# Kernel tuning notes

Hardware: AMD Instinct MI355X
Metric: run time of the kernel (lower is better)

The kernel has to match this reference:

```python
import jax, jax.numpy as jnp
import numpy as np

N_NODES = 100000
N_EDGES = 3200000
D_IN = 64
D_OUT = 64


def setup_inputs() -> dict:
    key = jax.random.key(0)
    k0, k1, k2, k3 = jax.random.split(key, 4)
    x = jax.random.normal(k0, (N_NODES, D_IN), dtype=jnp.float32)
    edge_index = jax.random.randint(k1, (2, N_EDGES), 0, N_NODES, dtype=jnp.int64)
    edge_weight = jax.random.uniform(k2, (N_EDGES,), dtype=jnp.float32)
    W = jax.random.normal(k3, (D_IN, D_OUT), dtype=jnp.float32) / jnp.sqrt(jnp.float32(D_IN))
    b = jnp.zeros((D_OUT,), dtype=jnp.float32)
    return {"x": x, "edge_index": edge_index, "edge_weight": edge_weight, "W": W, "b": b}


def reference(x, edge_index, edge_weight, W, b):
    # GiGCNConv forward: asymmetric (random-walk, D^-1 A) gcn_norm with self loops,
    # then GCNConv(normalize=False): linear -> edge-weighted scatter-add -> bias.
    N = x.shape[0]
    src, dst = edge_index[0], edge_index[1]

    # add self loops (fill value 1.0 since improved=False)
    loop = jnp.arange(N, dtype=src.dtype)
    src = jnp.concatenate([src, loop])
    dst = jnp.concatenate([dst, loop])
    ew = jnp.concatenate([edge_weight.astype(x.dtype), jnp.ones((N,), dtype=x.dtype)])

    # asymmetric normalization: in-degree (at dst) inverse scaling
    deg = jax.ops.segment_sum(ew, dst, num_segments=N)          # [N]
    deg_inv = jnp.where(deg > 0, 1.0 / deg, 0.0)                # inf -> 0
    norm = deg_inv[dst] * ew                                    # [E+N]

    # GCNConv: project then aggregate messages at destination nodes
    h = x @ W                                                   # [N, D_OUT]
    msg = norm[:, None] * h[src]                                # [E+N, D_OUT] gather
    out = jax.ops.segment_sum(msg, dst, num_segments=N)         # scatter-add
    return out + b
```

## Files before the change

kernel.cpp:

```cpp
#include <hip/hip_runtime.h>


#define D 64
#define BSH 9
#define NPB 512
#define MAXB1 256
#define BATCHA 4096
#define C1S 32
#define WSCALE 8192.0f
#define WINV (1.0f / 8192.0f)

static __device__ __forceinline__ unsigned short f2bf(float f) {
    unsigned u = __float_as_uint(f);
    u += 0x7FFFu + ((u >> 16) & 1u);
    return (unsigned short)(u >> 16);
}
static __device__ __forceinline__ float bflo(unsigned u) {
    return __uint_as_float(u << 16);
}
static __device__ __forceinline__ float bfhi(unsigned u) {
    return __uint_as_float(u & 0xFFFF0000u);
}


__global__ __launch_bounds__(256) void hist_kernel(const int* __restrict__ dst,
                                                   int* __restrict__ hist, int E, int B1) {
    __shared__ int lh[MAXB1];
    int tid = threadIdx.x;
    if (tid < MAXB1) lh[tid] = 0;
    __syncthreads();
    int t = blockIdx.x * 256 + tid;
    int stride = gridDim.x * 256;
    if ((E & 3) == 0 && (((size_t)dst & 15) == 0)) {
        const int4* d4 = (const int4*)dst;
        int n4 = E >> 2;
        for (int e = t; e < n4; e += stride) {
            int4 v = d4[e];
            atomicAdd(&lh[v.x >> BSH], 1);
            atomicAdd(&lh[v.y >> BSH], 1);
            atomicAdd(&lh[v.z >> BSH], 1);
            atomicAdd(&lh[v.w >> BSH], 1);
        }
    } else {
        for (int e = t; e < E; e += stride) {
            int d = __builtin_nontemporal_load(dst + e);
            atomicAdd(&lh[d >> BSH], 1);
        }
    }
    __syncthreads();
    if (tid < B1) {
        int v = lh[tid];
        if (v) atomicAdd(&hist[tid], v);
    }
}


__global__ __launch_bounds__(256) void scan_kernel(const int* __restrict__ hist,
                                                   int* __restrict__ off1,
                                                   int* __restrict__ cur1, int B1, int E) {
    __shared__ int s[256];
    int tid = threadIdx.x;
    int v = (tid < B1) ? hist[tid] : 0;
    s[tid] = v;
    __syncthreads();
    for (int o = 1; o < 256; o <<= 1) {
        int t = (tid >= o) ? s[tid - o] : 0;
        __syncthreads();
        s[tid] += t;
        __syncthreads();
    }
    if (tid < B1) {
        int ex = s[tid] - v;
        off1[tid] = ex;
        cur1[tid * C1S] = ex;
    }
    if (tid == 0) off1[B1] = E;
}


__global__ __launch_bounds__(256) void partA_kernel(const int* __restrict__ src,
                                                    const int* __restrict__ dst,
                                                    const float* __restrict__ ew,
                                                    int* __restrict__ cur1,
                                                    int2* __restrict__ pairs1,
                                                    int E, int nb, int aligned) {
    __shared__ int bcnt[MAXB1];
    __shared__ int bbase[MAXB1];
    __shared__ int brank[MAXB1];
    int tid = threadIdx.x;
    for (int ib = blockIdx.x; ib < nb; ib += gridDim.x) {
        int base = ib * BATCHA;
        int blen = E - base;
        if (blen > BATCHA) blen = BATCHA;
        if (tid < MAXB1) { bcnt[tid] = 0; brank[tid] = 0; }
        __syncthreads();
        int dv[16], sv[16];
        float wv[16];
        int off = tid * 16;
        if (aligned && off + 16 <= blen) {
#pragma unroll
            for (int kk = 0; kk < 4; ++kk) {
                int4 d4 = ((const int4*)(dst + base + off))[kk];
                int4 s4 = ((const int4*)(src + base + off))[kk];
                float4 w4 = ((const float4*)(ew + base + off))[kk];
                dv[kk * 4 + 0] = d4.x; dv[kk * 4 + 1] = d4.y;
                dv[kk * 4 + 2] = d4.z; dv[kk * 4 + 3] = d4.w;
                sv[kk * 4 + 0] = s4.x; sv[kk * 4 + 1] = s4.y;
                sv[kk * 4 + 2] = s4.z; sv[kk * 4 + 3] = s4.w;
                wv[kk * 4 + 0] = w4.x; wv[kk * 4 + 1] = w4.y;
                wv[kk * 4 + 2] = w4.z; wv[kk * 4 + 3] = w4.w;
            }
#pragma unroll
            for (int m = 0; m < 16; ++m) atomicAdd(&bcnt[dv[m] >> BSH], 1);
        } else {
#pragma unroll
            for (int m = 0; m < 16; ++m) {
                bool v = (off + m) < blen;
                int e = base + off + m;
                dv[m] = v ? __builtin_nontemporal_load(dst + e) : -1;
                sv[m] = v ? __builtin_nontemporal_load(src + e) : 0;
                wv[m] = v ? __builtin_nontemporal_load(ew + e) : 0.0f;
                if (v) atomicAdd(&bcnt[dv[m] >> BSH], 1);
            }
        }
        __syncthreads();
        if (tid < MAXB1 && bcnt[tid] > 0)
            bbase[tid] = atomicAdd(&cur1[tid * C1S], bcnt[tid]);
        __syncthreads();
#pragma unroll
        for (int m = 0; m < 16; ++m) {
            if (dv[m] >= 0) {
                int bin = dv[m] >> BSH;
                int r = atomicAdd(&brank[bin], 1);
                pairs1[bbase[bin] + r] =
                    make_int2(sv[m] | ((dv[m] & (NPB - 1)) << 17),
                              __float_as_int(wv[m]));
            }
        }
        __syncthreads();
    }
}


__global__ __launch_bounds__(512) void sortmerge_kernel(const int2* __restrict__ pairs1,
                                                        const int* __restrict__ off1,
                                                        unsigned* __restrict__ cw,
                                                        int* __restrict__ node_off,
                                                        int N, int B1) {
    __shared__ int lh[NPB];
    __shared__ int s[NPB];
    __shared__ int cur[NPB];
    int tid = threadIdx.x;
    int c = blockIdx.x;
    int e0 = off1[c], e1 = off1[c + 1];

    lh[tid] = 0;
    __syncthreads();

    for (int ib = e0; ib < e1; ib += 512 * 8) {
        long long pv[8];
#pragma unroll
        for (int m = 0; m < 8; ++m) {
            int i = ib + m * 512 + tid;
            pv[m] = (i < e1)
                ? __builtin_nontemporal_load((const long long*)(pairs1 + i))
                : -1LL;
        }
#pragma unroll
        for (int m = 0; m < 8; ++m) {
            int i = ib + m * 512 + tid;
            if (i < e1) atomicAdd(&lh[((int)pv[m] >> 17) & (NPB - 1)], 1);
        }
    }
    __syncthreads();

    s[tid] = lh[tid];
    __syncthreads();
    for (int o = 1; o < NPB; o <<= 1) {
        int t = (tid >= o) ? s[tid - o] : 0;
        __syncthreads();
        s[tid] += t;
        __syncthreads();
    }
    int ex = s[tid] - lh[tid];
    int gbase = c << BSH;
    if (gbase + tid <= N) node_off[gbase + tid] = e0 + ex;
    if (c == B1 - 1 && tid == 0) node_off[N] = e1;
    cur[tid] = ex;
    __syncthreads();

    for (int ib = e0; ib < e1; ib += 512 * 8) {
        long long pv[8];
#pragma unroll
        for (int m = 0; m < 8; ++m) {
            int i = ib + m * 512 + tid;
            pv[m] = (i < e1)
                ? __builtin_nontemporal_load((const long long*)(pairs1 + i))
                : -1LL;
        }
#pragma unroll
        for (int m = 0; m < 8; ++m) {
            int i = ib + m * 512 + tid;
            if (i < e1) {
                int px = (int)pv[m];
                float w = __int_as_float((int)(pv[m] >> 32));
                int node = (px >> 17) & (NPB - 1);
                int pos = atomicAdd(&cur[node], 1);
                int wq = (int)fminf(fmaxf(w, 0.0f) * WSCALE + 0.5f, 32767.0f);
                cw[e0 + pos] = (unsigned)(px & 0x1FFFF) | ((unsigned)wq << 17);
            }
        }
    }
}


__global__ __launch_bounds__(256) void gemmW_kernel(const float* __restrict__ x,
                                                    const float* __restrict__ W,
                                                    unsigned short* __restrict__ hbf, int N) {
    __shared__ float Ws[D * D];
    __shared__ float xs[32][D];
    int tid = threadIdx.x;
    int j = tid & 63;
    int g = tid >> 6;
    int base = blockIdx.x * 32;
    for (int i = tid; i < D * D; i += 256) Ws[i] = W[i];
    for (int rr = g; rr < 32; rr += 4) {
        int r = base + rr;
        if (r < N) xs[rr][j] = x[(size_t)r * D + j];
    }
    __syncthreads();
    float wc[D];
#pragma unroll
    for (int k = 0; k < D; ++k) wc[k] = Ws[k * D + j];
    for (int rr = g; rr < 32; rr += 4) {
        int r = base + rr;
        if (r < N) {
            float s0 = 0.0f, s1 = 0.0f, s2 = 0.0f, s3 = 0.0f;
#pragma unroll
            for (int k = 0; k < D; k += 4) {
                s0 = fmaf(xs[rr][k + 0], wc[k + 0], s0);
                s1 = fmaf(xs[rr][k + 1], wc[k + 1], s1);
                s2 = fmaf(xs[rr][k + 2], wc[k + 2], s2);
                s3 = fmaf(xs[rr][k + 3], wc[k + 3], s3);
            }
            hbf[(size_t)r * D + j] = f2bf((s0 + s1) + (s2 + s3));
        }
    }
}


__global__ __launch_bounds__(256) void accum_kernel(const unsigned* __restrict__ cw,
                                                    const int* __restrict__ node_off,
                                                    const unsigned short* __restrict__ hbf,
                                                    const float* __restrict__ bias,
                                                    float* __restrict__ out, int N) {
    int t = blockIdx.x * 256 + threadIdx.x;
    int n = t >> 6;
    int l = t & 63;
    if (n >= N) return;
    int eg = l >> 4;
    int cl = l & 15;
    int base = node_off[n];
    int cnt = node_off[n + 1] - base;
    const unsigned* pp = cw + base;
    const unsigned short* hcol = hbf + cl * 4;

    float a0 = 0.0f, a1 = 0.0f, a2 = 0.0f, a3 = 0.0f;
    float degs = 0.0f;
    int i = eg;
    for (; i + 12 < cnt; i += 16) {
        unsigned va = pp[i];
        unsigned vb = pp[i + 4];
        unsigned vc = pp[i + 8];
        unsigned vd = pp[i + 12];
        uint2 ha = *(const uint2*)(hcol + (size_t)(va & 0x1FFFF) * D);
        uint2 hb = *(const uint2*)(hcol + (size_t)(vb & 0x1FFFF) * D);
        uint2 hc = *(const uint2*)(hcol + (size_t)(vc & 0x1FFFF) * D);
        uint2 hd = *(const uint2*)(hcol + (size_t)(vd & 0x1FFFF) * D);
        float wa = (float)(va >> 17) * WINV;
        float wb = (float)(vb >> 17) * WINV;
        float wc = (float)(vc >> 17) * WINV;
        float wd = (float)(vd >> 17) * WINV;
        degs += (wa + wb) + (wc + wd);
        a0 = fmaf(wa, bflo(ha.x), a0);
        a1 = fmaf(wa, bfhi(ha.x), a1);
        a2 = fmaf(wa, bflo(ha.y), a2);
        a3 = fmaf(wa, bfhi(ha.y), a3);
        a0 = fmaf(wb, bflo(hb.x), a0);
        a1 = fmaf(wb, bfhi(hb.x), a1);
        a2 = fmaf(wb, bflo(hb.y), a2);
        a3 = fmaf(wb, bfhi(hb.y), a3);
        a0 = fmaf(wc, bflo(hc.x), a0);
        a1 = fmaf(wc, bfhi(hc.x), a1);
        a2 = fmaf(wc, bflo(hc.y), a2);
        a3 = fmaf(wc, bfhi(hc.y), a3);
        a0 = fmaf(wd, bflo(hd.x), a0);
        a1 = fmaf(wd, bfhi(hd.x), a1);
        a2 = fmaf(wd, bflo(hd.y), a2);
        a3 = fmaf(wd, bfhi(hd.y), a3);
    }
    for (; i < cnt; i += 4) {
        unsigned v = pp[i];
        uint2 hv = *(const uint2*)(hcol + (size_t)(v & 0x1FFFF) * D);
        float w = (float)(v >> 17) * WINV;
        degs += w;
        a0 = fmaf(w, bflo(hv.x), a0);
        a1 = fmaf(w, bfhi(hv.x), a1);
        a2 = fmaf(w, bflo(hv.y), a2);
        a3 = fmaf(w, bfhi(hv.y), a3);
    }

    a0 += __shfl_xor(a0, 16); a0 += __shfl_xor(a0, 32);
    a1 += __shfl_xor(a1, 16); a1 += __shfl_xor(a1, 32);
    a2 += __shfl_xor(a2, 16); a2 += __shfl_xor(a2, 32);
    a3 += __shfl_xor(a3, 16); a3 += __shfl_xor(a3, 32);
    degs += __shfl_xor(degs, 16); degs += __shfl_xor(degs, 32);

    if (eg == 0) {
        uint2 hs = *(const uint2*)(hcol + (size_t)n * D);
        a0 += bflo(hs.x);
        a1 += bfhi(hs.x);
        a2 += bflo(hs.y);
        a3 += bfhi(hs.y);
        degs += 1.0f;
        float di = 1.0f / degs;
        const float4 bv = *(const float4*)(bias + cl * 4);
        float4 o;
        o.x = fmaf(di, a0, bv.x);
        o.y = fmaf(di, a1, bv.y);
        o.z = fmaf(di, a2, bv.z);
        o.w = fmaf(di, a3, bv.w);
        __builtin_nontemporal_store(o.x, out + (size_t)n * D + cl * 4 + 0);
        __builtin_nontemporal_store(o.y, out + (size_t)n * D + cl * 4 + 1);
        __builtin_nontemporal_store(o.z, out + (size_t)n * D + cl * 4 + 2);
        __builtin_nontemporal_store(o.w, out + (size_t)n * D + cl * 4 + 3);
    }
}


__global__ __launch_bounds__(256) void deg_kernel(const int* __restrict__ dst,
                                                  const float* __restrict__ ew,
                                                  float* __restrict__ deg, int E) {
    int t = blockIdx.x * 256 + threadIdx.x;
    int stride = gridDim.x * 256;
    for (int e = t; e < E; e += stride) atomicAdd(&deg[dst[e]], ew[e]);
}

__global__ __launch_bounds__(256) void deginv_kernel(float* __restrict__ deg, int N) {
    int t = blockIdx.x * 256 + threadIdx.x;
    int stride = gridDim.x * 256;
    for (int n = t; n < N; n += stride) {
        float tot = deg[n] + 1.0f;
        deg[n] = (tot > 0.0f) ? (1.0f / tot) : 0.0f;
    }
}

__global__ __launch_bounds__(256) void gemm16f_kernel(const float* __restrict__ x,
                                                      const float* __restrict__ W,
                                                      float* __restrict__ h, int N) {
    __shared__ float Ws[D * D];
    __shared__ float xs[16][D];
    int tid = threadIdx.x;
    int j = tid & 63;
    int q = tid >> 6;
    int base = blockIdx.x * 16;
    for (int i = tid; i < D * D; i += 256) Ws[i] = W[i];
    for (int rr = q; rr < 16; rr += 4) {
        int r = base + rr;
        if (r < N) xs[rr][j] = x[(size_t)r * D + j];
    }
    __syncthreads();
    for (int rr = q; rr < 16; rr += 4) {
        int r = base + rr;
        if (r < N) {
            float sum = 0.0f;
#pragma unroll
            for (int k = 0; k < D; ++k) sum = fmaf(xs[rr][k], Ws[k * D + j], sum);
            h[(size_t)r * D + j] = sum;
        }
    }
}

__global__ __launch_bounds__(256) void init_kernel(const float* __restrict__ h,
                                                   const float* __restrict__ deginv,
                                                   const float* __restrict__ b,
                                                   float* __restrict__ out, int N) {
    int t = blockIdx.x * 256 + threadIdx.x;
    int stride = gridDim.x * 256;
    int nq = N * (D / 4);
    const float4* h4 = (const float4*)h;
    const float4* b4 = (const float4*)b;
    float4* o4 = (float4*)out;
    for (int q = t; q < nq; q += stride) {
        int n = q >> 4;
        int c4 = q & 15;
        float4 hv = h4[q];
        float4 bv = b4[c4];
        float di = deginv[n];
        float4 o;
        o.x = bv.x + di * hv.x;
        o.y = bv.y + di * hv.y;
        o.z = bv.z + di * hv.z;
        o.w = bv.w + di * hv.w;
        o4[q] = o;
    }
}

__global__ __launch_bounds__(256) void scatter_kernel(const int* __restrict__ src,
                                                      const int* __restrict__ dst,
                                                      const float* __restrict__ ew,
                                                      const float* __restrict__ deginv,
                                                      const float* __restrict__ h,
                                                      float* __restrict__ out, int E) {
    int t = blockIdx.x * 256 + threadIdx.x;
    int wave = t >> 6;
    int lane = t & 63;
    int nwaves = (gridDim.x * 256) >> 6;
    for (int e = wave; e < E; e += nwaves) {
        int s = src[e];
        int d = dst[e];
        float norm = deginv[d] * ew[e];
        atomicAdd(&out[d * D + lane], norm * h[s * D + lane]);
    }
}


extern "C" void kernel_launch(void* const* d_in, const int* in_sizes, int n_in,
                              void* d_out, int out_size, void* d_ws, size_t ws_size,
                              hipStream_t stream) {
    const float* x  = (const float*)d_in[0];
    const int*   ei = (const int*)d_in[1];
    const float* ew = (const float*)d_in[2];
    const float* W  = (const float*)d_in[3];
    const float* b  = (const float*)d_in[4];
    float* out = (float*)d_out;

    int N = in_sizes[0] / D;
    int E = in_sizes[2];
    const int* srcp = ei;
    const int* dstp = ei + E;

    int B1 = (N + NPB - 1) >> BSH;

    size_t ints_n = 256 + 320 + (size_t)MAXB1 * C1S + ((size_t)N + 64);
    size_t p1_off  = ((ints_n * 4) + 255) & ~(size_t)255;
    size_t hbf_off = (p1_off + (size_t)E * 8 + 255) & ~(size_t)255;
    size_t cw_off  = (hbf_off + (size_t)N * D * 2 + 255) & ~(size_t)255;
    size_t need = cw_off + (size_t)E * 4;

    if (N <= 131072 && ws_size >= need) {
        int* hist     = (int*)d_ws;
        int* off1     = hist + 256;
        int* cur1     = off1 + 320;
        int* node_off = cur1 + (size_t)MAXB1 * C1S;
        int2* pairs1  = (int2*)((char*)d_ws + p1_off);
        unsigned short* hbf = (unsigned short*)((char*)d_ws + hbf_off);
        unsigned* cw  = (unsigned*)((char*)d_ws + cw_off);

        int aligned = (((E & 3) == 0) && (((size_t)dstp & 15) == 0)) ? 1 : 0;

        hipMemsetAsync(hist, 0, 256 * 4, stream);
        hist_kernel<<<512, 256, 0, stream>>>(dstp, hist, E, B1);
        scan_kernel<<<1, 256, 0, stream>>>(hist, off1, cur1, B1, E);
        int nb = (E + BATCHA - 1) / BATCHA;
        int gA = nb < 2048 ? nb : 2048;
        partA_kernel<<<gA, 256, 0, stream>>>(srcp, dstp, ew, cur1, pairs1, E, nb, aligned);
        sortmerge_kernel<<<B1, 512, 0, stream>>>(pairs1, off1, cw, node_off, N, B1);
        gemmW_kernel<<<(N + 31) / 32, 256, 0, stream>>>(x, W, hbf, N);
        accum_kernel<<<(N + 3) / 4, 256, 0, stream>>>(cw, node_off, hbf, b, out, N);
    } else {
        size_t Npad = ((size_t)N + 63) & ~(size_t)63;
        float* deg = (float*)d_ws;
        float* h = deg + Npad;
        hipMemsetAsync(deg, 0, (size_t)N * sizeof(float), stream);
        deg_kernel<<<2048, 256, 0, stream>>>(dstp, ew, deg, E);
        deginv_kernel<<<(N + 255) / 256, 256, 0, stream>>>(deg, N);
        gemm16f_kernel<<<(N + 15) / 16, 256, 0, stream>>>(x, W, h, N);
        init_kernel<<<2048, 256, 0, stream>>>(h, deg, b, out, N);
        scatter_kernel<<<2048, 256, 0, stream>>>(srcp, dstp, ew, deg, h, out, E);
    }
}
```

Baseline: 183.1 us.

## Merge edge partition and X·W GEMM into one heterogeneous launch

```diff
diff --git a/kernel.cpp b/kernel.cpp
--- a/kernel.cpp
+++ b/kernel.cpp
@@ -78,66 +78,101 @@
 }
 
 
-__global__ __launch_bounds__(256) void partA_kernel(const int* __restrict__ src,
-                                                    const int* __restrict__ dst,
-                                                    const float* __restrict__ ew,
-                                                    int* __restrict__ cur1,
-                                                    int2* __restrict__ pairs1,
-                                                    int E, int nb, int aligned) {
-    __shared__ int bcnt[MAXB1];
-    __shared__ int bbase[MAXB1];
-    __shared__ int brank[MAXB1];
+__global__ __launch_bounds__(256) void partgemm_kernel(const int* __restrict__ src,
+                                                       const int* __restrict__ dst,
+                                                       const float* __restrict__ ew,
+                                                       int* __restrict__ cur1,
+                                                       int2* __restrict__ pairs1,
+                                                       int E, int nb, int aligned, int gA,
+                                                       const float* __restrict__ x,
+                                                       const float* __restrict__ W,
+                                                       unsigned short* __restrict__ hbf,
+                                                       int N) {
+    __shared__ union SM {
+        struct { int bcnt[MAXB1]; int bbase[MAXB1]; int brank[MAXB1]; } p;
+        struct { float Ws[D * D]; float xs[32][D]; } g;
+    } sm;
     int tid = threadIdx.x;
-    for (int ib = blockIdx.x; ib < nb; ib += gridDim.x) {
-        int base = ib * BATCHA;
-        int blen = E - base;
-        if (blen > BATCHA) blen = BATCHA;
-        if (tid < MAXB1) { bcnt[tid] = 0; brank[tid] = 0; }
+
+    if ((int)blockIdx.x < gA) {
+        for (int ib = blockIdx.x; ib < nb; ib += gA) {
+            int base = ib * BATCHA;
+            int blen = E - base;
+            if (blen > BATCHA) blen = BATCHA;
+            if (tid < MAXB1) { sm.p.bcnt[tid] = 0; sm.p.brank[tid] = 0; }
+            __syncthreads();
+            int dv[16], sv[16];
+            float wv[16];
+            int off = tid * 16;
+            if (aligned && off + 16 <= blen) {
+#pragma unroll
+                for (int kk = 0; kk < 4; ++kk) {
+                    int4 d4 = ((const int4*)(dst + base + off))[kk];
+                    int4 s4 = ((const int4*)(src + base + off))[kk];
+                    float4 w4 = ((const float4*)(ew + base + off))[kk];
+                    dv[kk * 4 + 0] = d4.x; dv[kk * 4 + 1] = d4.y;
+                    dv[kk * 4 + 2] = d4.z; dv[kk * 4 + 3] = d4.w;
+                    sv[kk * 4 + 0] = s4.x; sv[kk * 4 + 1] = s4.y;
+                    sv[kk * 4 + 2] = s4.z; sv[kk * 4 + 3] = s4.w;
+                    wv[kk * 4 + 0] = w4.x; wv[kk * 4 + 1] = w4.y;
+                    wv[kk * 4 + 2] = w4.z; wv[kk * 4 + 3] = w4.w;
+                }
+#pragma unroll
+                for (int m = 0; m < 16; ++m) atomicAdd(&sm.p.bcnt[dv[m] >> BSH], 1);
+            } else {
+#pragma unroll
+                for (int m = 0; m < 16; ++m) {
+                    bool v = (off + m) < blen;
+                    int e = base + off + m;
+                    dv[m] = v ? __builtin_nontemporal_load(dst + e) : -1;
+                    sv[m] = v ? __builtin_nontemporal_load(src + e) : 0;
+                    wv[m] = v ? __builtin_nontemporal_load(ew + e) : 0.0f;
+                    if (v) atomicAdd(&sm.p.bcnt[dv[m] >> BSH], 1);
+                }
+            }
+            __syncthreads();
+            if (tid < MAXB1 && sm.p.bcnt[tid] > 0)
+                sm.p.bbase[tid] = atomicAdd(&cur1[tid * C1S], sm.p.bcnt[tid]);
+            __syncthreads();
+#pragma unroll
+            for (int m = 0; m < 16; ++m) {
+                if (dv[m] >= 0) {
+                    int bin = dv[m] >> BSH;
+                    int r = atomicAdd(&sm.p.brank[bin], 1);
+                    pairs1[sm.p.bbase[bin] + r] =
+                        make_int2(sv[m] | ((dv[m] & (NPB - 1)) << 17),
+                                  __float_as_int(wv[m]));
+                }
+            }
+            __syncthreads();
+        }
+    } else {
+        int j = tid & 63;
+        int g = tid >> 6;
+        int base = ((int)blockIdx.x - gA) * 32;
+        for (int i = tid; i < D * D; i += 256) sm.g.Ws[i] = W[i];
+        for (int rr = g; rr < 32; rr += 4) {
+            int r = base + rr;
+            if (r < N) sm.g.xs[rr][j] = x[(size_t)r * D + j];
+        }
         __syncthreads();
-        int dv[16], sv[16];
-        float wv[16];
-        int off = tid * 16;
-        if (aligned && off + 16 <= blen) {
-#pragma unroll
-            for (int kk = 0; kk < 4; ++kk) {
-                int4 d4 = ((const int4*)(dst + base + off))[kk];
-                int4 s4 = ((const int4*)(src + base + off))[kk];
-                float4 w4 = ((const float4*)(ew + base + off))[kk];
-                dv[kk * 4 + 0] = d4.x; dv[kk * 4 + 1] = d4.y;
-                dv[kk * 4 + 2] = d4.z; dv[kk * 4 + 3] = d4.w;
-                sv[kk * 4 + 0] = s4.x; sv[kk * 4 + 1] = s4.y;
-                sv[kk * 4 + 2] = s4.z; sv[kk * 4 + 3] = s4.w;
-                wv[kk * 4 + 0] = w4.x; wv[kk * 4 + 1] = w4.y;
-                wv[kk * 4 + 2] = w4.z; wv[kk * 4 + 3] = w4.w;
+        float wc[D];
+#pragma unroll
+        for (int k = 0; k < D; ++k) wc[k] = sm.g.Ws[k * D + j];
+        for (int rr = g; rr < 32; rr += 4) {
+            int r = base + rr;
+            if (r < N) {
+                float s0 = 0.0f, s1 = 0.0f, s2 = 0.0f, s3 = 0.0f;
+#pragma unroll
+                for (int k = 0; k < D; k += 4) {
+                    s0 = fmaf(sm.g.xs[rr][k + 0], wc[k + 0], s0);
+                    s1 = fmaf(sm.g.xs[rr][k + 1], wc[k + 1], s1);
+                    s2 = fmaf(sm.g.xs[rr][k + 2], wc[k + 2], s2);
+                    s3 = fmaf(sm.g.xs[rr][k + 3], wc[k + 3], s3);
+                }
+                hbf[(size_t)r * D + j] = f2bf((s0 + s1) + (s2 + s3));
             }
-#pragma unroll
-            for (int m = 0; m < 16; ++m) atomicAdd(&bcnt[dv[m] >> BSH], 1);
-        } else {
-#pragma unroll
-            for (int m = 0; m < 16; ++m) {
-                bool v = (off + m) < blen;
-                int e = base + off + m;
-                dv[m] = v ? __builtin_nontemporal_load(dst + e) : -1;
-                sv[m] = v ? __builtin_nontemporal_load(src + e) : 0;
-                wv[m] = v ? __builtin_nontemporal_load(ew + e) : 0.0f;
-                if (v) atomicAdd(&bcnt[dv[m] >> BSH], 1);
-            }
-        }
-        __syncthreads();
-        if (tid < MAXB1 && bcnt[tid] > 0)
-            bbase[tid] = atomicAdd(&cur1[tid * C1S], bcnt[tid]);
-        __syncthreads();
-#pragma unroll
-        for (int m = 0; m < 16; ++m) {
-            if (dv[m] >= 0) {
-                int bin = dv[m] >> BSH;
-                int r = atomicAdd(&brank[bin], 1);
-                pairs1[bbase[bin] + r] =
-                    make_int2(sv[m] | ((dv[m] & (NPB - 1)) << 17),
-                              __float_as_int(wv[m]));
-            }
-        }
-        __syncthreads();
+        }
     }
 }
 
@@ -209,41 +244,6 @@
                 int wq = (int)fminf(fmaxf(w, 0.0f) * WSCALE + 0.5f, 32767.0f);
                 cw[e0 + pos] = (unsigned)(px & 0x1FFFF) | ((unsigned)wq << 17);
             }
-        }
-    }
-}
-
-
-__global__ __launch_bounds__(256) void gemmW_kernel(const float* __restrict__ x,
-                                                    const float* __restrict__ W,
-                                                    unsigned short* __restrict__ hbf, int N) {
-    __shared__ float Ws[D * D];
-    __shared__ float xs[32][D];
-    int tid = threadIdx.x;
-    int j = tid & 63;
-    int g = tid >> 6;
-    int base = blockIdx.x * 32;
-    for (int i = tid; i < D * D; i += 256) Ws[i] = W[i];
-    for (int rr = g; rr < 32; rr += 4) {
-        int r = base + rr;
-        if (r < N) xs[rr][j] = x[(size_t)r * D + j];
-    }
-    __syncthreads();
-    float wc[D];
-#pragma unroll
-    for (int k = 0; k < D; ++k) wc[k] = Ws[k * D + j];
-    for (int rr = g; rr < 32; rr += 4) {
-        int r = base + rr;
-        if (r < N) {
-            float s0 = 0.0f, s1 = 0.0f, s2 = 0.0f, s3 = 0.0f;
-#pragma unroll
-            for (int k = 0; k < D; k += 4) {
-                s0 = fmaf(xs[rr][k + 0], wc[k + 0], s0);
-                s1 = fmaf(xs[rr][k + 1], wc[k + 1], s1);
-                s2 = fmaf(xs[rr][k + 2], wc[k + 2], s2);
-                s3 = fmaf(xs[rr][k + 3], wc[k + 3], s3);
-            }
-            hbf[(size_t)r * D + j] = f2bf((s0 + s1) + (s2 + s3));
         }
     }
 }
@@ -464,9 +464,10 @@
         scan_kernel<<<1, 256, 0, stream>>>(hist, off1, cur1, B1, E);
         int nb = (E + BATCHA - 1) / BATCHA;
         int gA = nb < 2048 ? nb : 2048;
-        partA_kernel<<<gA, 256, 0, stream>>>(srcp, dstp, ew, cur1, pairs1, E, nb, aligned);
+        int gG = (N + 31) / 32;
+        partgemm_kernel<<<gA + gG, 256, 0, stream>>>(srcp, dstp, ew, cur1, pairs1,
+                                                     E, nb, aligned, gA, x, W, hbf, N);
         sortmerge_kernel<<<B1, 512, 0, stream>>>(pairs1, off1, cw, node_off, N, B1);
-        gemmW_kernel<<<(N + 31) / 32, 256, 0, stream>>>(x, W, hbf, N);
         accum_kernel<<<(N + 3) / 4, 256, 0, stream>>>(cw, node_off, hbf, b, out, N);
     } else {
         size_t Npad = ((size_t)N + 63) & ~(size_t)63;
```

Result: no change. 180.3 us (-1.5%).
